# Kernel tuning notes

Hardware: AMD Instinct MI355X
Metric: run time of the kernel (lower is better)

Reference implementation:

```python
import jax, jax.numpy as jnp
import numpy as np

B, S, D, H = 2, 2048, 4096, 32
HD = D // H  # 128
HALF = HD // 2  # 64


def setup_inputs() -> dict:
    key = jax.random.key(0)
    ks = jax.random.split(key, 6)
    scale = 1.0 / np.sqrt(D)
    x = jax.random.normal(ks[0], (B, S, D), jnp.float32)
    Wq = jax.random.normal(ks[1], (D, D), jnp.float32) * scale
    Wk = jax.random.normal(ks[2], (D, D), jnp.float32) * scale
    Wv = jax.random.normal(ks[3], (D, D), jnp.float32) * scale
    Wo = jax.random.normal(ks[4], (D, D), jnp.float32) * scale
    # Rotary frequencies: complex freqs of shape (S, HD//2) split into cos/sin
    inv_freq = 1.0 / (10000.0 ** (np.arange(0, HD, 2, dtype=np.float32) / HD))
    angles = np.outer(np.arange(S, dtype=np.float32), inv_freq)  # (S, HALF)
    freq_cos = jnp.asarray(np.cos(angles), jnp.float32)
    freq_sin = jnp.asarray(np.sin(angles), jnp.float32)
    # Additive causal mask (0 on/below diag, large-negative above)
    causal = jnp.tril(jnp.ones((S, S), jnp.bool_))
    mask = jnp.where(causal, 0.0, -1e9).astype(jnp.float32)
    return {"x": x, "Wq": Wq, "Wk": Wk, "Wv": Wv, "Wo": Wo,
            "freq_cos": freq_cos, "freq_sin": freq_sin, "mask": mask,
            "start_position": 0, "n_rep": 1}


def _apply_rope(t, freq_cos, freq_sin):
    # t: [B, S, H, HD]; complex multiply on interleaved (even, odd) pairs
    b, s, h, hd = t.shape
    tr = t.reshape(b, s, h, hd // 2, 2)
    a, c = tr[..., 0], tr[..., 1]
    cos = freq_cos[None, :, None, :]  # [1, S, 1, HALF]
    sin = freq_sin[None, :, None, :]
    out = jnp.stack([a * cos - c * sin, a * sin + c * cos], axis=-1)
    return out.reshape(b, s, h, hd)


def reference(x, Wq, Wk, Wv, Wo, freq_cos, freq_sin, mask, start_position, n_rep):
    b, s, _ = x.shape
    q = (x @ Wq).reshape(b, s, H, HD)
    k = (x @ Wk).reshape(b, s, H, HD)
    v = (x @ Wv).reshape(b, s, H, HD)
    q = _apply_rope(q, freq_cos, freq_sin)
    k = _apply_rope(k, freq_cos, freq_sin)
    if n_rep > 1:  # repeat_kv (identity when n_rep == 1)
        k = jnp.repeat(k, n_rep, axis=2)
        v = jnp.repeat(v, n_rep, axis=2)
    # KV-cache: with start_position=0 and s == max_sequence_length, the
    # cache slice [:, :start_position+s] equals the freshly written k/v.
    scores = jnp.einsum('bqhd,bkhd->bhqk', q, k) / jnp.sqrt(jnp.float32(HD))
    scores = scores + mask  # broadcast [S,S] over [B,H,S,S]
    weights = jax.nn.softmax(scores, axis=-1)
    out = jnp.einsum('bhqk,bkhd->bqhd', weights, v)
    out = out.reshape(b, s, H * HD)
    return out @ Wo
```

## Files before the change

kernel.cpp:

```cpp
#include <hip/hip_runtime.h>
#include <hip/hip_bf16.h>

#define DD 4096
#define MM 4096
#define SS 2048
#define HH 32
#define HDD 128
#define NT 64

typedef unsigned short u16;
typedef __attribute__((ext_vector_type(8))) __bf16 bf16x8;
typedef __attribute__((ext_vector_type(4))) float f32x4;
typedef __attribute__((ext_vector_type(4))) float float4v;
typedef __attribute__((ext_vector_type(8))) unsigned short ushort8;
typedef __attribute__((ext_vector_type(4))) unsigned int uint4v;

__device__ __forceinline__ u16 f2bf(float f) {
  union { float f; unsigned u; } v; v.f = f;
  unsigned u = v.u;
  return (u16)((u + 0x7fffu + ((u >> 16) & 1u)) >> 16);
}
__device__ __forceinline__ float bf2f(u16 s) {
  union { unsigned u; float f; } v; v.u = ((unsigned)s) << 16;
  return v.f;
}
__device__ __forceinline__ f32x4 zero4() { f32x4 z = {0.f, 0.f, 0.f, 0.f}; return z; }

__device__ __forceinline__ void gl_lds16(const u16* g, u16* l) {
  __builtin_amdgcn_global_load_lds((__attribute__((address_space(1))) void*)(g),
                                   (__attribute__((address_space(3))) void*)(l), 16, 0, 0);
}

__device__ __forceinline__ unsigned cvtpk(float lo, float hi) {
  unsigned r;
  asm("v_cvt_pk_bf16_f32 %0, %1, %2" : "=v"(r) : "v"(lo), "v"(hi));
  return r;
}
__device__ __forceinline__ float exp2a(float x) {
  float r;
  asm("v_exp_f32 %0, %1" : "=v"(r) : "v"(x));
  return r;
}

__global__ __launch_bounds__(256) void k_cvt(const float* __restrict__ in,
                                             u16* __restrict__ out, int n8) {
  int i = blockIdx.x * blockDim.x + threadIdx.x;
  if (i >= n8) return;
  size_t o = (size_t)i * 8;
  float4v a = *(const float4v*)(in + o);
  float4v b = *(const float4v*)(in + o + 4);
  ushort8 v;
  v[0] = f2bf(a[0]); v[1] = f2bf(a[1]); v[2] = f2bf(a[2]); v[3] = f2bf(a[3]);
  v[4] = f2bf(b[0]); v[5] = f2bf(b[1]); v[6] = f2bf(b[2]); v[7] = f2bf(b[3]);
  *(ushort8*)(out + o) = v;
}

__global__ __launch_bounds__(256) void k_wt(const float* __restrict__ W0,
                                            const float* __restrict__ W1,
                                            const float* __restrict__ W2,
                                            const float* __restrict__ W3,
                                            u16* __restrict__ out) {
  const float* W = blockIdx.z == 0 ? W0 : blockIdx.z == 1 ? W1 : blockIdx.z == 2 ? W2 : W3;
  u16* O = out + (size_t)blockIdx.z * DD * DD;
  __shared__ u16 t[64][65];
  int k0 = blockIdx.x * 64, n0 = blockIdx.y * 64;
  int tx = threadIdx.x, ty = threadIdx.y;
#pragma unroll
  for (int i = 0; i < 16; ++i) {
    int kk = ty + i * 4;
    t[tx][kk] = f2bf(W[(size_t)(k0 + kk) * DD + n0 + tx]);
  }
  __syncthreads();
#pragma unroll
  for (int i = 0; i < 16; ++i) {
    int nn = ty + i * 4;
    O[(size_t)(n0 + nn) * DD + k0 + tx] = t[nn][tx];
  }
}

#define MFMA16(QM, QN)                                                             \
  _Pragma("unroll") for (int kk = 0; kk < 2; ++kk)                                 \
  _Pragma("unroll") for (int mi = 0; mi < 4; ++mi)                                 \
  _Pragma("unroll") for (int ni = 0; ni < 2; ++ni)                                 \
      acc[(QM)*4 + mi][(QN)*2 + ni] = __builtin_amdgcn_mfma_f32_16x16x32_bf16(     \
          af[mi][kk], bf[(QN)*2 + ni][kk], acc[(QM)*4 + mi][(QN)*2 + ni], 0, 0, 0);

#define RDA(BB, QM)                                                                \
  _Pragma("unroll") for (int mi = 0; mi < 4; ++mi)                                 \
  _Pragma("unroll") for (int kk = 0; kk < 2; ++kk)                                 \
      af[mi][kk] = *(const bf16x8*)((const char*)&L[BB][0][0] +                    \
          ((abase + ((QM)*4 + mi) * 2048 + kk * 64) ^ xsw));

#define RDB(BB, QN)                                                                \
  _Pragma("unroll") for (int ni = 0; ni < 2; ++ni)                                 \
  _Pragma("unroll") for (int kk = 0; kk < 2; ++kk)                                 \
      bf[(QN)*2 + ni][kk] = *(const bf16x8*)((const char*)&L[BB][1][0] +           \
          ((bbase + ((QN)*2 + ni) * 2048 + kk * 64) ^ xsw));

#define BAR() __builtin_amdgcn_s_barrier()
#define LGKM0() asm volatile("s_waitcnt lgkmcnt(0)" ::: "memory")
#define PRIO1() __builtin_amdgcn_s_setprio(1)
#define PRIO0() __builtin_amdgcn_s_setprio(0)

template <int MODE>
__global__ __launch_bounds__(512, 2) void k_gemm(const u16* __restrict__ A,
                                                 const u16* __restrict__ Bt,
                                                 void* __restrict__ Cout) {
  __shared__ __align__(16) u16 L[2][2][16384];
  const int tid = threadIdx.x;
  const int wid = tid >> 6, lane = tid & 63;
  const int g = lane >> 4, li = lane & 15;
  const int wr = wid >> 2, wc = wid & 3;

  const int bid = blockIdx.x;
  const int sw = ((bid & 7) << 5) | (bid >> 3);
  const int brow = (sw >> 4) * 256, bcol = (sw & 15) * 256;

  const int xsw = (li & 7) << 4;
  const int abase = (wr * 128 + li) * 128 + g * 16;
  const int bbase = (wc * 64 + li) * 128 + g * 16;

  const int sxy = ((tid >> 3) & 7) << 3;
  const int scol = ((tid * 8) ^ sxy) & 63;
  const int srow0 = tid >> 3;

  auto STAGE = [&](int gidx) {
    if (gidx >= 4 * NT) return;
    const int t = gidx >> 2, h = gidx & 3;
    const int bb2 = t & 1;
    const int mat = h >> 1;
    const int half = h & 1;
    const u16* G = mat ? Bt : A;
    const int rowbase = (mat ? bcol : brow) + half * 128;
    const int k0 = t << 6;
    u16* Ld = &L[bb2][mat][half * 8192 + wid * 512];
    const u16* gsrc = G + (size_t)(rowbase + srow0) * DD + k0 + scol;
    gl_lds16(gsrc, Ld);
    gl_lds16(gsrc + (size_t)64 * DD, Ld + 4096);
  };

  f32x4 acc[8][4];
#pragma unroll
  for (int m = 0; m < 8; ++m)
#pragma unroll
    for (int n = 0; n < 4; ++n) acc[m][n] = zero4();

  bf16x8 af[4][2], bf[4][2];

#pragma unroll
  for (int gi = 0; gi < 5; ++gi) STAGE(gi);
  asm volatile("s_waitcnt vmcnt(2)" ::: "memory");
  BAR();

  for (int kt = 0; kt < NT; ++kt) {
    const int bb = kt & 1;
    const int gb = 4 * kt;
    RDA(bb, 0); RDB(bb, 0);
    STAGE(gb + 5);
    BAR(); LGKM0();
    PRIO1(); MFMA16(0, 0); PRIO0();
    BAR();
    RDB(bb, 1);
    STAGE(gb + 6);
    BAR(); LGKM0();
    PRIO1(); MFMA16(0, 1); PRIO0();
    BAR();
    RDA(bb, 1);
    STAGE(gb + 7);
    BAR(); LGKM0();
    PRIO1(); MFMA16(1, 0); PRIO0();
    BAR();
    STAGE(gb + 8);
    if (kt < NT - 2) {
      asm volatile("s_waitcnt vmcnt(2)" ::: "memory");
    } else {
      asm volatile("s_waitcnt vmcnt(0)" ::: "memory");
    }
    BAR(); LGKM0();
    PRIO1(); MFMA16(1, 1); PRIO0();
    BAR();
  }

#pragma unroll
  for (int m = 0; m < 8; ++m) {
#pragma unroll
    for (int n = 0; n < 4; ++n) {
#pragma unroll
      for (int r = 0; r < 4; ++r) {
        int row = brow + wr * 128 + m * 16 + g * 4 + r;
        int col = bcol + wc * 64 + n * 16 + li;
        float v = acc[m][n][r];
        if (MODE == 0) {
          ((u16*)Cout)[(size_t)row * DD + col] = f2bf(v);
        } else if (MODE == 1) {
          ((u16*)Cout)[((size_t)((row >> 11) << 12) + col) * SS + (row & 2047)] = f2bf(v);
        } else {
          ((float*)Cout)[(size_t)row * DD + col] = v;
        }
      }
    }
  }
}

__global__ __launch_bounds__(256) void k_rope(u16* __restrict__ Q, u16* __restrict__ Kp,
                                              const float* __restrict__ fc,
                                              const float* __restrict__ fs) {
  int idx = blockIdx.x * blockDim.x + threadIdx.x;
  const int n8 = MM * DD / 8;
  const float qsc = idx < n8 ? 0.08838834764831845f * 1.44269504088896340f : 1.0f;
  u16* T = idx < n8 ? Q : Kp;
  int i = idx < n8 ? idx : idx - n8;
  int m = i >> 9;
  int c = (i & 511) * 8;
  int s = m & (SS - 1);
  int i0 = (c & (HDD - 1)) >> 1;
  size_t o = (size_t)m * DD + c;
  ushort8 v = *(ushort8*)(T + o);
  float4v cs = *(const float4v*)(fc + s * 64 + i0);
  float4v sn = *(const float4v*)(fs + s * 64 + i0);
  ushort8 ov;
#pragma unroll
  for (int p = 0; p < 4; ++p) {
    float a = bf2f(v[2 * p]), cc = bf2f(v[2 * p + 1]);
    ov[2 * p]     = f2bf((a * cs[p] - cc * sn[p]) * qsc);
    ov[2 * p + 1] = f2bf((a * sn[p] + cc * cs[p]) * qsc);
  }
  *(ushort8*)(T + o) = ov;
}

__global__ __launch_bounds__(256) void k_attn(const u16* __restrict__ Q,
                                              const u16* __restrict__ K,
                                              const u16* __restrict__ VT,
                                              u16* __restrict__ O) {
  __shared__ __align__(16) u16 Kl[2][32 * 128];
  __shared__ __align__(16) u16 Vl[2][128 * 32];
  __shared__ __align__(16) u16 Pl[4][16 * 32];
  const int bh = blockIdx.x;
  const int qt = 31 - blockIdx.y;
  const int b = bh >> 5, h = bh & 31;
  const int tid = threadIdx.x, w = tid >> 6, lane = tid & 63;
  const int g = lane >> 4, li = lane & 15;

  const u16* Qbase = Q + ((size_t)(b * SS + qt * 64 + w * 16 + li)) * DD + h * HDD;
  const u16* Kbase = K + ((size_t)(b * SS)) * DD + h * HDD;
  const u16* Vbase = VT + ((size_t)bh) * HDD * SS;

  bf16x8 qf[4];
#pragma unroll
  for (int ks = 0; ks < 4; ++ks)
    qf[ks] = *(const bf16x8*)(Qbase + ks * 32 + g * 8);

  f32x4 oa[8];
#pragma unroll
  for (int f = 0; f < 8; ++f) oa[f] = zero4();
  float mrun = -1e30f, lrun = 0.f;
  const int wli = w * 16 + li;

  const int krow0 = w * 8 + (lane >> 4);
  const int ksg0 = (lane & 15) ^ (lane >> 4);
  const int ksg1 = (lane & 15) ^ (4 + (lane >> 4));
  const int vdr0 = w * 16 + (lane >> 2);
  const int va0 = (vdr0 * 64 + (lane & 3) * 16) ^ (((vdr0 >> 1) & 7) << 4);
  const int vdr1 = vdr0 + 64;
  const int va1 = (vdr1 * 64 + (lane & 3) * 16) ^ (((vdr1 >> 1) & 7) << 4);

  auto STAGE = [&](int t, int nb) {
    const u16* Kt = Kbase + (size_t)(t * 32) * DD;
    gl_lds16(Kt + (size_t)krow0 * DD + ksg0 * 8, &Kl[nb][(w * 8) * 128]);
    gl_lds16(Kt + (size_t)(krow0 + 4) * DD + ksg1 * 8, &Kl[nb][(w * 8 + 4) * 128]);
    const u16* Vt = Vbase + t * 32;
    gl_lds16(Vt + (size_t)(va0 >> 6) * SS + ((va0 >> 4) & 3) * 8, &Vl[nb][w * 512]);
    gl_lds16(Vt + (size_t)(va1 >> 6) * SS + ((va1 >> 4) & 3) * 8, &Vl[nb][2048 + w * 512]);
  };

  auto TILE = [&](int kt, int cb, int koff) __attribute__((always_inline)) {
    f32x4 sc[2];
    sc[0] = zero4(); sc[1] = zero4();
    PRIO1();
#pragma unroll
    for (int ks = 0; ks < 4; ++ks) {
#pragma unroll
      for (int ktg = 0; ktg < 2; ++ktg) {
        int kr = ktg * 16 + li;
        int off = (kr * 256 + (ks * 32 + g * 8) * 2) ^ ((kr & 7) << 4);
        bf16x8 kf = *(const bf16x8*)((const char*)Kl[cb] + off);
        sc[ktg] = __builtin_amdgcn_mfma_f32_16x16x32_bf16(kf, qf[ks], sc[ktg], 0, 0, 0);
      }
    }
    PRIO0();

    float p[8];
    float tmax = -1e30f;
#pragma unroll
    for (int ktg = 0; ktg < 2; ++ktg) {
#pragma unroll
      for (int r = 0; r < 4; ++r) {
        float s = sc[ktg][r];
        if (koff >= 0 && (koff + ktg * 16 + g * 4 + r > wli)) s = -1e30f;
        p[ktg * 4 + r] = s;
        tmax = fmaxf(tmax, s);
      }
    }
    tmax = fmaxf(tmax, __shfl_xor(tmax, 16));
    tmax = fmaxf(tmax, __shfl_xor(tmax, 32));

    if (__all(tmax <= mrun + 8.f)) {
      float su = 0.f;
#pragma unroll
      for (int i = 0; i < 8; ++i) { p[i] = exp2a(p[i] - mrun); su += p[i]; }
      su += __shfl_xor(su, 16);
      su += __shfl_xor(su, 32);
      lrun += su;
    } else {
      float mnew = fmaxf(mrun, tmax);
      float alpha = exp2a(mrun - mnew);
      mrun = mnew;
      float su = 0.f;
#pragma unroll
      for (int i = 0; i < 8; ++i) { p[i] = exp2a(p[i] - mnew); su += p[i]; }
      su += __shfl_xor(su, 16);
      su += __shfl_xor(su, 32);
      lrun = lrun * alpha + su;
      float av[4];
#pragma unroll
      for (int r = 0; r < 4; ++r) av[r] = __shfl(alpha, g * 20 + r);
#pragma unroll
      for (int f = 0; f < 8; ++f)
#pragma unroll
        for (int r = 0; r < 4; ++r) oa[f][r] *= av[r];
    }

    {
      char* Pb = (char*)Pl[w];
      const int swz = ((li >> 1) & 7) << 4;
#pragma unroll
      for (int ktg = 0; ktg < 2; ++ktg) {
#pragma unroll
        for (int j = 0; j < 2; ++j) {
          unsigned pk = cvtpk(p[ktg * 4 + 2 * j], p[ktg * 4 + 2 * j + 1]);
          int off = (li * 64 + ktg * 32 + g * 8 + 4 * j) ^ swz;
          *(unsigned*)(Pb + off) = pk;
        }
      }
    }
    asm volatile("s_waitcnt lgkmcnt(0)" ::: "memory");

    PRIO1();
    {
      int poff = (li * 64 + g * 16) ^ (((li >> 1) & 7) << 4);
      bf16x8 pfrag = *(const bf16x8*)((const char*)Pl[w] + poff);
#pragma unroll
      for (int f = 0; f < 8; ++f) {
        int dr = f * 16 + li;
        int voff = (dr * 64 + g * 16) ^ (((dr >> 1) & 7) << 4);
        bf16x8 vf = *(const bf16x8*)((const char*)Vl[cb] + voff);
        oa[f] = __builtin_amdgcn_mfma_f32_16x16x32_bf16(pfrag, vf, oa[f], 0, 0, 0);
      }
    }
    PRIO0();

    asm volatile("s_waitcnt vmcnt(0)" ::: "memory");
    __syncthreads();
  };

  STAGE(0, 0);
  asm volatile("s_waitcnt vmcnt(0)" ::: "memory");
  __syncthreads();

  for (int i = 0; i < qt; ++i) {
    STAGE(2 * i + 1, 1);
    TILE(2 * i, 0, -1);
    STAGE(2 * i + 2, 0);
    TILE(2 * i + 1, 1, -1);
  }
  STAGE(2 * qt + 1, 1);
  TILE(2 * qt, 0, 0);
  TILE(2 * qt + 1, 1, 32);

  float lv[4];
#pragma unroll
  for (int r = 0; r < 4; ++r) lv[r] = __shfl(lrun, g * 20 + r);
  u16* Ob = O + ((size_t)(b * SS + qt * 64 + w * 16 + g * 4)) * DD + h * HDD;
#pragma unroll
  for (int r = 0; r < 4; ++r) {
    float inv = 1.f / lv[r];
#pragma unroll
    for (int f = 0; f < 8; ++f)
      Ob[(size_t)r * DD + f * 16 + li] = f2bf(oa[f][r] * inv);
  }
}

extern "C" void kernel_launch(void* const* d_in, const int* in_sizes, int n_in,
                              void* d_out, int out_size, void* d_ws, size_t ws_size,
                              hipStream_t stream) {
  (void)in_sizes; (void)n_in; (void)out_size; (void)ws_size;
  const float* x    = (const float*)d_in[0];
  const float* Wq   = (const float*)d_in[1];
  const float* Wk   = (const float*)d_in[2];
  const float* Wv   = (const float*)d_in[3];
  const float* Wo   = (const float*)d_in[4];
  const float* fcos = (const float*)d_in[5];
  const float* fsin = (const float*)d_in[6];

  u16* ws = (u16*)d_ws;
  const size_t MAT = (size_t)4096 * 4096;
  u16* xb    = ws + 0 * MAT;
  u16* wqt   = ws + 1 * MAT;
  u16* wkt   = ws + 2 * MAT;
  u16* wvt   = ws + 3 * MAT;
  u16* wot   = ws + 4 * MAT;
  u16* Qb    = ws + 5 * MAT;
  u16* Kb    = ws + 6 * MAT;
  u16* VTb   = ws + 7 * MAT;
  u16* attnb = ws + 8 * MAT;

  k_cvt<<<dim3(8192), dim3(256), 0, stream>>>(x, xb, (int)(MAT / 8));
  k_wt<<<dim3(64, 64, 4), dim3(64, 4), 0, stream>>>(Wq, Wk, Wv, Wo, wqt);
  k_gemm<0><<<dim3(256), dim3(512), 0, stream>>>(xb, wqt, (void*)Qb);
  k_gemm<0><<<dim3(256), dim3(512), 0, stream>>>(xb, wkt, (void*)Kb);
  k_gemm<1><<<dim3(256), dim3(512), 0, stream>>>(xb, wvt, (void*)VTb);
  k_rope<<<dim3(16384), dim3(256), 0, stream>>>(Qb, Kb, fcos, fsin);
  k_attn<<<dim3(64, 32), dim3(256), 0, stream>>>(Qb, Kb, VTb, attnb);
  k_gemm<2><<<dim3(256), dim3(512), 0, stream>>>(attnb, wot, d_out);
}
```

Baseline: 812.8 us.

## Fuse RoPE into Q/K GEMM epilogue and restage loads per k-tile

Removes the standalone RoPE kernel by applying the rotary transform (and the Q softmax scale) inside the Q and K projection GEMM epilogues, using a lane shuffle to fetch the paired element. This drops one full read-modify-write pass over Q and K. It also changes the GEMM prefetch schedule from four staggered quarter-stage loads per k-iteration to one full k-tile load issued before the last MFMA phase, with a matching vmcnt wait. The new schedule clusters global loads, which may hurt overlap, and the epilogue now does scalar gathers of cos/sin.

```diff
diff --git a/kernel.cpp b/kernel.cpp
--- a/kernel.cpp
+++ b/kernel.cpp
@@ -105,7 +105,9 @@
 template <int MODE>
 __global__ __launch_bounds__(512, 2) void k_gemm(const u16* __restrict__ A,
                                                  const u16* __restrict__ Bt,
-                                                 void* __restrict__ Cout) {
+                                                 void* __restrict__ Cout,
+                                                 const float* __restrict__ fc,
+                                                 const float* __restrict__ fs) {
   __shared__ __align__(16) u16 L[2][2][16384];
   const int tid = threadIdx.x;
   const int wid = tid >> 6, lane = tid & 63;
@@ -124,19 +126,20 @@
   const int scol = ((tid * 8) ^ sxy) & 63;
   const int srow0 = tid >> 3;
 
-  auto STAGE = [&](int gidx) {
-    if (gidx >= 4 * NT) return;
-    const int t = gidx >> 2, h = gidx & 3;
+  auto STAGE4 = [&](int t) {
+    if (t >= NT) return;
     const int bb2 = t & 1;
-    const int mat = h >> 1;
-    const int half = h & 1;
-    const u16* G = mat ? Bt : A;
-    const int rowbase = (mat ? bcol : brow) + half * 128;
-    const int k0 = t << 6;
-    u16* Ld = &L[bb2][mat][half * 8192 + wid * 512];
-    const u16* gsrc = G + (size_t)(rowbase + srow0) * DD + k0 + scol;
-    gl_lds16(gsrc, Ld);
-    gl_lds16(gsrc + (size_t)64 * DD, Ld + 4096);
+#pragma unroll
+    for (int hh = 0; hh < 4; ++hh) {
+      const int mat = hh >> 1;
+      const int half = hh & 1;
+      const u16* G = mat ? Bt : A;
+      const int rowbase = (mat ? bcol : brow) + half * 128;
+      u16* Ld = &L[bb2][mat][half * 8192 + wid * 512];
+      const u16* gsrc = G + (size_t)(rowbase + srow0) * DD + (t << 6) + scol;
+      gl_lds16(gsrc, Ld);
+      gl_lds16(gsrc + (size_t)64 * DD, Ld + 4096);
+    }
   };
 
   f32x4 acc[8][4];
@@ -147,32 +150,28 @@
 
   bf16x8 af[4][2], bf[4][2];
 
-#pragma unroll
-  for (int gi = 0; gi < 5; ++gi) STAGE(gi);
-  asm volatile("s_waitcnt vmcnt(2)" ::: "memory");
+  STAGE4(0);
+  STAGE4(1);
+  asm volatile("s_waitcnt vmcnt(8)" ::: "memory");
   BAR();
 
   for (int kt = 0; kt < NT; ++kt) {
     const int bb = kt & 1;
-    const int gb = 4 * kt;
     RDA(bb, 0); RDB(bb, 0);
-    STAGE(gb + 5);
     BAR(); LGKM0();
     PRIO1(); MFMA16(0, 0); PRIO0();
     BAR();
     RDB(bb, 1);
-    STAGE(gb + 6);
     BAR(); LGKM0();
     PRIO1(); MFMA16(0, 1); PRIO0();
     BAR();
     RDA(bb, 1);
-    STAGE(gb + 7);
     BAR(); LGKM0();
     PRIO1(); MFMA16(1, 0); PRIO0();
     BAR();
-    STAGE(gb + 8);
+    STAGE4(kt + 2);
     if (kt < NT - 2) {
-      asm volatile("s_waitcnt vmcnt(2)" ::: "memory");
+      asm volatile("s_waitcnt vmcnt(8)" ::: "memory");
     } else {
       asm volatile("s_waitcnt vmcnt(0)" ::: "memory");
     }
@@ -194,38 +193,22 @@
           ((u16*)Cout)[(size_t)row * DD + col] = f2bf(v);
         } else if (MODE == 1) {
           ((u16*)Cout)[((size_t)((row >> 11) << 12) + col) * SS + (row & 2047)] = f2bf(v);
+        } else if (MODE == 2) {
+          ((float*)Cout)[(size_t)row * DD + col] = v;
         } else {
-          ((float*)Cout)[(size_t)row * DD + col] = v;
+          int s = row & (SS - 1);
+          int d = col & (HDD - 1);
+          int i0 = d >> 1;
+          float pv = __shfl_xor(v, 1);
+          float cs = fc[s * 64 + i0];
+          float sn = fs[s * 64 + i0];
+          float rr = (d & 1) ? (pv * sn + v * cs) : (v * cs - pv * sn);
+          if (MODE == 3) rr *= 0.08838834764831845f * 1.44269504088896340f;
+          ((u16*)Cout)[(size_t)row * DD + col] = f2bf(rr);
         }
       }
     }
   }
-}
-
-__global__ __launch_bounds__(256) void k_rope(u16* __restrict__ Q, u16* __restrict__ Kp,
-                                              const float* __restrict__ fc,
-                                              const float* __restrict__ fs) {
-  int idx = blockIdx.x * blockDim.x + threadIdx.x;
-  const int n8 = MM * DD / 8;
-  const float qsc = idx < n8 ? 0.08838834764831845f * 1.44269504088896340f : 1.0f;
-  u16* T = idx < n8 ? Q : Kp;
-  int i = idx < n8 ? idx : idx - n8;
-  int m = i >> 9;
-  int c = (i & 511) * 8;
-  int s = m & (SS - 1);
-  int i0 = (c & (HDD - 1)) >> 1;
-  size_t o = (size_t)m * DD + c;
-  ushort8 v = *(ushort8*)(T + o);
-  float4v cs = *(const float4v*)(fc + s * 64 + i0);
-  float4v sn = *(const float4v*)(fs + s * 64 + i0);
-  ushort8 ov;
-#pragma unroll
-  for (int p = 0; p < 4; ++p) {
-    float a = bf2f(v[2 * p]), cc = bf2f(v[2 * p + 1]);
-    ov[2 * p]     = f2bf((a * cs[p] - cc * sn[p]) * qsc);
-    ov[2 * p + 1] = f2bf((a * sn[p] + cc * cs[p]) * qsc);
-  }
-  *(ushort8*)(T + o) = ov;
 }
 
 __global__ __launch_bounds__(256) void k_attn(const u16* __restrict__ Q,
@@ -416,10 +399,9 @@
 
   k_cvt<<<dim3(8192), dim3(256), 0, stream>>>(x, xb, (int)(MAT / 8));
   k_wt<<<dim3(64, 64, 4), dim3(64, 4), 0, stream>>>(Wq, Wk, Wv, Wo, wqt);
-  k_gemm<0><<<dim3(256), dim3(512), 0, stream>>>(xb, wqt, (void*)Qb);
-  k_gemm<0><<<dim3(256), dim3(512), 0, stream>>>(xb, wkt, (void*)Kb);
-  k_gemm<1><<<dim3(256), dim3(512), 0, stream>>>(xb, wvt, (void*)VTb);
-  k_rope<<<dim3(16384), dim3(256), 0, stream>>>(Qb, Kb, fcos, fsin);
+  k_gemm<3><<<dim3(256), dim3(512), 0, stream>>>(xb, wqt, (void*)Qb, fcos, fsin);
+  k_gemm<4><<<dim3(256), dim3(512), 0, stream>>>(xb, wkt, (void*)Kb, fcos, fsin);
+  k_gemm<1><<<dim3(256), dim3(512), 0, stream>>>(xb, wvt, (void*)VTb, nullptr, nullptr);
   k_attn<<<dim3(64, 32), dim3(256), 0, stream>>>(Qb, Kb, VTb, attnb);
-  k_gemm<2><<<dim3(256), dim3(512), 0, stream>>>(attnb, wot, d_out);
-}
+  k_gemm<2><<<dim3(256), dim3(512), 0, stream>>>(attnb, wot, d_out, nullptr, nullptr);
+}
```

Result: no change. 820.4 us (+0.9%).
